# Kernel optimization log

Measured on AMD Instinct MI355X. Metric: run time of the kernel, lower is better.

## Reference

```python
import jax, jax.numpy as jnp
import numpy as np

N_NODES = 100000


def setup_inputs() -> dict:
    key = jax.random.key(0)
    k1, k2, k3 = jax.random.split(key, 3)
    feat = jax.random.normal(k1, (N_NODES, 64), dtype=jnp.float32)
    src = jax.random.randint(k2, (1250000,), 0, N_NODES, dtype=jnp.int64)
    dst = jax.random.randint(k3, (1250000,), 0, N_NODES, dtype=jnp.int64)
    return {"feat": feat, "src": src, "dst": dst}


def reference(feat, src, dst):
    # GraphConv(norm='both', activation=None): degree-normalized neighbor sum
    # with implicit self-connection (rst = feat_dst + sum_neighbors), where
    # degrees are clamp(min=1) + 1 to account for the self edge.
    n = feat.shape[0]
    ones = jnp.ones(src.shape[0], dtype=feat.dtype)
    out_deg = jax.ops.segment_sum(ones, src, num_segments=n)
    in_deg = jax.ops.segment_sum(ones, dst, num_segments=n)
    norm_l = jax.lax.rsqrt(jnp.maximum(out_deg, 1.0) + 1.0)  # [N]
    norm_r = jax.lax.rsqrt(jnp.maximum(in_deg, 1.0) + 1.0)   # [N]
    feat_src = feat * norm_l[:, None]                         # left-normalize
    msgs = feat_src[src]                                      # gather [E, D]
    h_neigh = jax.ops.segment_sum(msgs, dst, num_segments=n)  # scatter-sum [N, D]
    rst = (feat + h_neigh) * norm_r[:, None]                  # right-normalize
    return rst
```

## Files before the change

kernel.cpp:

```cpp
#include <hip/hip_runtime.h>


#define GC_D 64
#define PSIZE 196
#define SCAP 3072
#define EPT 12
#define EPB (512*EPT)
#define MAXPART 512
#define GC_CAP 64


__global__ __launch_bounds__(512) void partition_kernel(
        const int* __restrict__ src,
        const int* __restrict__ dst,
        int* __restrict__ curA,
        int* __restrict__ curB,
        int* __restrict__ streamA,
        unsigned char* __restrict__ streamB,
        int e, int nPart) {
    __shared__ int histA[MAXPART], histB[MAXPART], baseA[MAXPART], baseB[MAXPART];
    __shared__ int lofsA[MAXPART];
    __shared__ int sval[EPB];
    __shared__ unsigned short sbin[EPB];
    int t = threadIdx.x;
    for (int i = t; i < nPart; i += 512) { histA[i] = 0; histB[i] = 0; }
    __syncthreads();
    int lo = blockIdx.x * EPB;
    int base_i = lo + t * EPT;
    int se[EPT], de[EPT], rkA[EPT], rkB[EPT];
    bool aligned16 = ((((size_t)src) | ((size_t)dst)) & 15) == 0;
    if (aligned16 && base_i + EPT <= e) {
        int4 s0 = *(const int4*)(src + base_i);
        int4 s1 = *(const int4*)(src + base_i + 4);
        int4 s2 = *(const int4*)(src + base_i + 8);
        int4 d0 = *(const int4*)(dst + base_i);
        int4 d1 = *(const int4*)(dst + base_i + 4);
        int4 d2 = *(const int4*)(dst + base_i + 8);
        se[0]=s0.x; se[1]=s0.y; se[2]=s0.z; se[3]=s0.w;
        se[4]=s1.x; se[5]=s1.y; se[6]=s1.z; se[7]=s1.w;
        se[8]=s2.x; se[9]=s2.y; se[10]=s2.z; se[11]=s2.w;
        de[0]=d0.x; de[1]=d0.y; de[2]=d0.z; de[3]=d0.w;
        de[4]=d1.x; de[5]=d1.y; de[6]=d1.z; de[7]=d1.w;
        de[8]=d2.x; de[9]=d2.y; de[10]=d2.z; de[11]=d2.w;
#pragma unroll
        for (int k = 0; k < EPT; ++k) {
            rkA[k] = atomicAdd(&histA[de[k] / PSIZE], 1);
            rkB[k] = atomicAdd(&histB[se[k] / PSIZE], 1);
        }
    } else {
#pragma unroll
        for (int k = 0; k < EPT; ++k) {
            int i = base_i + k;
            se[k] = 0; de[k] = 0; rkA[k] = 0; rkB[k] = 0;
            if (i < e) {
                se[k] = src[i]; de[k] = dst[i];
                rkA[k] = atomicAdd(&histA[de[k] / PSIZE], 1);
                rkB[k] = atomicAdd(&histB[se[k] / PSIZE], 1);
            }
        }
    }
    __syncthreads();
    for (int i = t; i < nPart; i += 512) {
        int hA = histA[i];
        baseA[i] = hA ? atomicAdd(&curA[i], hA) : 0;
        int hB = histB[i];
        baseB[i] = hB ? atomicAdd(&curB[i], hB) : 0;
    }
    lofsA[t] = (t < nPart) ? histA[t] : 0;
    __syncthreads();
    for (int off = 1; off < MAXPART; off <<= 1) {
        int a = (t >= off) ? lofsA[t - off] : 0;
        __syncthreads();
        lofsA[t] += a;
        __syncthreads();
    }
#pragma unroll
    for (int k = 0; k < EPT; ++k) {
        int i = base_i + k;
        if (i < e) {
            int s = se[k], d = de[k];
            int pA = d / PSIZE;
            int slot = lofsA[pA] - histA[pA] + rkA[k];
            sval[slot] = s | ((d - pA * PSIZE) << 17);
            sbin[slot] = (unsigned short)pA;
            int pB = s / PSIZE;
            int posB = baseB[pB] + rkB[k];
            if (posB < SCAP) streamB[pB * SCAP + posB] = (unsigned char)(s - pB * PSIZE);
        }
    }
    __syncthreads();
    int nE = min(EPB, e - lo);
    for (int i = t; i < nE; i += 512) {
        int bin = sbin[i];
        int pos = baseA[bin] + (i - (lofsA[bin] - histA[bin]));
        if (pos < SCAP) streamA[bin * SCAP + pos] = sval[i];
    }
}

__device__ __forceinline__ unsigned short to_bf16_rne(float v) {
    unsigned b = __float_as_uint(v);
    b = (b + 0x7FFFu + ((b >> 16) & 1u)) >> 16;
    return (unsigned short)b;
}

__global__ __launch_bounds__(512) void convertB_kernel(
        const int* __restrict__ curB,
        const unsigned char* __restrict__ streamB,
        const float* __restrict__ feat,
        unsigned short* __restrict__ featb,
        int n) {
    __shared__ int lodeg[256];
    __shared__ float lnl[256];
    int p = blockIdx.x, t = threadIdx.x;
    if (t < 256) lodeg[t] = 0;
    __syncthreads();
    int cB = min(curB[p], SCAP);
    const unsigned char* sB = streamB + (size_t)p * SCAP;
    for (int i = t; i < cB; i += 512) atomicAdd(&lodeg[sB[i]], 1);
    __syncthreads();
    if (t < 256) lnl[t] = rsqrtf(fmaxf((float)lodeg[t], 1.0f) + 1.0f);
    __syncthreads();
    int g = p * PSIZE;
    for (int q = t; q < PSIZE * 16; q += 512) {
        int r = q >> 4;
        int node = g + r;
        if (node >= n) break;
        float nl = lnl[r];
        size_t base = (size_t)node * GC_D + (q & 15) * 4;
        const float4 v = *(const float4*)(feat + base);
        ushort4 rr;
        rr.x = to_bf16_rne(v.x * nl);
        rr.y = to_bf16_rne(v.y * nl);
        rr.z = to_bf16_rne(v.z * nl);
        rr.w = to_bf16_rne(v.w * nl);
        *(ushort4*)(featb + base) = rr;
    }
    if (p == 0 && t < GC_D) featb[(size_t)n * GC_D + t] = 0;
}

__global__ __launch_bounds__(1024) void sortgather_kernel(
        const int* __restrict__ curA,
        const int* __restrict__ streamA,
        const float* __restrict__ feat,
        const unsigned short* __restrict__ featb,
        float* __restrict__ out,
        int n) {
    __shared__ int lperm[SCAP];
    __shared__ int lcnt[256], loff[256];
    int p = blockIdx.x, t = threadIdx.x;
    if (t < 256) lcnt[t] = 0;
    __syncthreads();
    int cA = min(curA[p], SCAP);
    const int* sA = streamA + (size_t)p * SCAP;
    int vv[3], rk[3];
#pragma unroll
    for (int it = 0; it < 3; ++it) {
        int i = it * 1024 + t;
        vv[it] = 0; rk[it] = -1;
        if (i < cA) {
            int v = sA[i];
            vv[it] = v;
            rk[it] = atomicAdd(&lcnt[(v >> 17) & 255], 1);
        }
    }
    __syncthreads();
    if (t < 256) loff[t] = lcnt[t];
    __syncthreads();
    for (int off = 1; off < 256; off <<= 1) {
        int a = (t < 256 && t >= off) ? loff[t - off] : 0;
        __syncthreads();
        if (t < 256) loff[t] += a;
        __syncthreads();
    }
    if (t < 256) loff[t] -= lcnt[t];
    __syncthreads();
#pragma unroll
    for (int it = 0; it < 3; ++it) {
        if (rk[it] >= 0) {
            int v = vv[it];
            lperm[loff[(v >> 17) & 255] + rk[it]] = v & 0x1FFFF;
        }
    }
    __syncthreads();
    int wave = t >> 6, lane = t & 63;
    int half = lane >> 5;
    int c = lane & 31;
    int g = p * PSIZE;
    for (int r = wave; r < PSIZE; r += 16) {
        int node = g + r;
        if (node >= n) break;
        int deg = lcnt[r];
        int off = loff[r];
        float acc0 = 0.0f, acc1 = 0.0f;
        for (int base = 0; base < deg; base += 64) {
            int m = min(deg - base, 64);
            int s_l = (lane < m) ? lperm[off + base + lane] : n;
            int m16 = (m + 15) & ~15;
            for (int j = 0; j < m16; j += 16) {
#pragma unroll
                for (int k = 0; k < 8; ++k) {
                    int s = __shfl(s_l, j + 2 * k + half);
                    unsigned u = *(const unsigned*)(featb + (size_t)s * GC_D + 2 * c);
                    acc0 += __uint_as_float(u << 16);
                    acc1 += __uint_as_float(u & 0xFFFF0000u);
                }
            }
        }
        acc0 += __shfl_xor(acc0, 32);
        acc1 += __shfl_xor(acc1, 32);
        if (half == 0) {
            float nr = rsqrtf(fmaxf((float)deg, 1.0f) + 1.0f);
            const float2 self = *(const float2*)(feat + (size_t)node * GC_D + 2 * c);
            float2 rr;
            rr.x = (self.x + acc0) * nr;
            rr.y = (self.y + acc1) * nr;
            *(float2*)(out + (size_t)node * GC_D + 2 * c) = rr;
        }
    }
}


__global__ void zero_int_kernel(int* __restrict__ p, int n) {
    int i = blockIdx.x * blockDim.x + threadIdx.x;
    if (i < n) p[i] = 0;
}

__global__ void bucket_hist_kernel(const int* __restrict__ src,
                                   const int* __restrict__ dst,
                                   int* __restrict__ cnt,
                                   int* __restrict__ outdeg,
                                   int* __restrict__ bucket,
                                   int e) {
    int i = blockIdx.x * blockDim.x + threadIdx.x;
    if (i < e) {
        int s = src[i];
        int d = dst[i];
        atomicAdd(&outdeg[s], 1);
        int pos = atomicAdd(&cnt[d], 1);
        if (pos < GC_CAP) bucket[d * GC_CAP + pos] = s;
    }
}

__global__ __launch_bounds__(256) void convert_kernel(
        const float* __restrict__ feat,
        const int* __restrict__ outdeg,
        unsigned short* __restrict__ featb,
        int n) {
    int i = blockIdx.x * 256 + threadIdx.x;
    int row = i >> 4;
    if (row > n) return;
    if (row == n) {
        ushort4 z; z.x = 0; z.y = 0; z.z = 0; z.w = 0;
        *(ushort4*)(featb + (size_t)i * 4) = z;
        return;
    }
    float nl = rsqrtf(fmaxf((float)outdeg[row], 1.0f) + 1.0f);
    float4 v = *(const float4*)(feat + (size_t)i * 4);
    ushort4 r;
    r.x = to_bf16_rne(v.x * nl);
    r.y = to_bf16_rne(v.y * nl);
    r.z = to_bf16_rne(v.z * nl);
    r.w = to_bf16_rne(v.w * nl);
    *(ushort4*)(featb + (size_t)i * 4) = r;
}

__global__ __launch_bounds__(256) void gather_bf16_kernel(
        const float* __restrict__ feat,
        const unsigned short* __restrict__ featb,
        const int* __restrict__ bucket,
        const int* __restrict__ cnt,
        float* __restrict__ out,
        int n) {
    int wid = (blockIdx.x * blockDim.x + threadIdx.x) >> 6;
    int lane = threadIdx.x & 63;
    if (wid >= n) return;
    int deg = cnt[wid];
    int s_raw = bucket[wid * GC_CAP + lane];
    int m = min(deg, GC_CAP);
    int s_l = (lane < m) ? s_raw : n;
    int half = lane >> 5;
    int c = lane & 31;
    float acc0 = 0.0f, acc1 = 0.0f;
    int m16 = (m + 15) & ~15;
    for (int j = 0; j < m16; j += 16) {
#pragma unroll
        for (int k = 0; k < 8; ++k) {
            int s = __shfl(s_l, j + 2 * k + half);
            unsigned u = *(const unsigned*)(featb + (size_t)s * GC_D + 2 * c);
            acc0 += __uint_as_float(u << 16);
            acc1 += __uint_as_float(u & 0xFFFF0000u);
        }
    }
    acc0 += __shfl_xor(acc0, 32);
    acc1 += __shfl_xor(acc1, 32);
    if (half == 0) {
        float nr = rsqrtf(fmaxf((float)deg, 1.0f) + 1.0f);
        const float2 self = *(const float2*)(feat + (size_t)wid * GC_D + 2 * c);
        float2 r;
        r.x = (self.x + acc0) * nr;
        r.y = (self.y + acc1) * nr;
        *(float2*)(out + (size_t)wid * GC_D + 2 * c) = r;
    }
}


extern "C" void kernel_launch(void* const* d_in, const int* in_sizes, int n_in,
                              void* d_out, int out_size, void* d_ws, size_t ws_size,
                              hipStream_t stream) {
    const float* feat = (const float*)d_in[0];
    const int*   src  = (const int*)d_in[1];
    const int*   dst  = (const int*)d_in[2];
    float* out = (float*)d_out;

    const int n = in_sizes[0] / GC_D;
    const int e = in_sizes[1];
    const int nPart = (n + PSIZE - 1) / PSIZE;

    size_t featb_ints = ((size_t)(n + 1) * GC_D + 1) / 2;
    size_t o = 2 * (size_t)nPart;
    o = (o + 31) & ~(size_t)31;
    size_t streamA_o = o;  o += (size_t)nPart * SCAP;
    size_t featb_o = o;    o += featb_ints;
    size_t need_main = o * sizeof(int) + (size_t)nPart * SCAP;

    size_t featb_bytes = (size_t)(n + 1) * GC_D * sizeof(unsigned short);
    size_t need_bf16 = ((size_t)2 * n + (size_t)n * GC_CAP) * sizeof(int) + featb_bytes;

    bool main_ok = (ws_size >= need_main) && nPart <= MAXPART && n <= 131071;

    if (main_ok) {
        int* ws = (int*)d_ws;
        int* curA = ws;
        int* curB = ws + nPart;
        int* streamA = ws + streamA_o;
        unsigned short* featb = (unsigned short*)(ws + featb_o);
        unsigned char* streamB = (unsigned char*)(ws + o);

        hipMemsetAsync(curA, 0, 2 * (size_t)nPart * sizeof(int), stream);
        partition_kernel<<<(e + EPB - 1) / EPB, 512, 0, stream>>>(
            src, dst, curA, curB, streamA, streamB, e, nPart);
        convertB_kernel<<<nPart, 512, 0, stream>>>(curB, streamB, feat, featb, n);
        sortgather_kernel<<<nPart, 1024, 0, stream>>>(curA, streamA, feat, featb,
                                                      out, n);
    } else if (ws_size >= need_bf16) {
        int* cnt    = (int*)d_ws;
        int* outdeg = cnt + n;
        int* bucket = outdeg + n;
        unsigned short* featb = (unsigned short*)(bucket + (size_t)n * GC_CAP);

        zero_int_kernel<<<(2 * n + 255) / 256, 256, 0, stream>>>(cnt, 2 * n);
        bucket_hist_kernel<<<(e + 255) / 256, 256, 0, stream>>>(src, dst, cnt,
                                                                outdeg, bucket, e);
        int conv_threads = (n + 1) * 16;
        convert_kernel<<<(conv_threads + 255) / 256, 256, 0, stream>>>(
            feat, outdeg, featb, n);
        long long total = (long long)n * GC_D;
        gather_bf16_kernel<<<(int)((total + 255) / 256), 256, 0, stream>>>(
            feat, featb, bucket, cnt, out, n);
    }
}
```

Measured before the change: 139.8 us.

## Split bf16 feature table into four column slabs for cache-local gathers

Stores the normalized bf16 features as four slabs of 16 columns (32 bytes per node) instead of interleaved 128-byte rows. The gather kernel loops over slabs, so each pass touches a table a quarter the size, which is meant to fit better in L2/MALL. Each wave now handles 8 edges per load step with 8 lanes per edge. The cost is re-reading the edge permutation four times, narrower 32-byte gathers, and a longer shuffle reduction.

```diff
diff --git a/kernel.cpp b/kernel.cpp
--- a/kernel.cpp
+++ b/kernel.cpp
@@ -121,21 +121,26 @@
     if (t < 256) lnl[t] = rsqrtf(fmaxf((float)lodeg[t], 1.0f) + 1.0f);
     __syncthreads();
     int g = p * PSIZE;
+    const size_t slabStride = (size_t)(n + 1) * 16;
     for (int q = t; q < PSIZE * 16; q += 512) {
         int r = q >> 4;
         int node = g + r;
         if (node >= n) break;
         float nl = lnl[r];
-        size_t base = (size_t)node * GC_D + (q & 15) * 4;
-        const float4 v = *(const float4*)(feat + base);
+        int quad = q & 15;
+        const float4 v = *(const float4*)(feat + (size_t)node * GC_D + quad * 4);
         ushort4 rr;
         rr.x = to_bf16_rne(v.x * nl);
         rr.y = to_bf16_rne(v.y * nl);
         rr.z = to_bf16_rne(v.z * nl);
         rr.w = to_bf16_rne(v.w * nl);
-        *(ushort4*)(featb + base) = rr;
-    }
-    if (p == 0 && t < GC_D) featb[(size_t)n * GC_D + t] = 0;
+        *(ushort4*)(featb + (size_t)(quad >> 2) * slabStride
+                    + (size_t)node * 16 + (quad & 3) * 4) = rr;
+    }
+    if (p == 0 && t < GC_D) {
+        int s = t >> 4, col = t & 15;
+        featb[(size_t)s * slabStride + (size_t)n * 16 + col] = 0;
+    }
 }
 
 __global__ __launch_bounds__(1024) void sortgather_kernel(
@@ -183,38 +188,41 @@
     }
     __syncthreads();
     int wave = t >> 6, lane = t & 63;
-    int half = lane >> 5;
-    int c = lane & 31;
+    int eg = lane >> 3;
+    int cp = lane & 7;
     int g = p * PSIZE;
-    for (int r = wave; r < PSIZE; r += 16) {
-        int node = g + r;
-        if (node >= n) break;
-        int deg = lcnt[r];
-        int off = loff[r];
-        float acc0 = 0.0f, acc1 = 0.0f;
-        for (int base = 0; base < deg; base += 64) {
-            int m = min(deg - base, 64);
-            int s_l = (lane < m) ? lperm[off + base + lane] : n;
-            int m16 = (m + 15) & ~15;
-            for (int j = 0; j < m16; j += 16) {
-#pragma unroll
-                for (int k = 0; k < 8; ++k) {
-                    int s = __shfl(s_l, j + 2 * k + half);
-                    unsigned u = *(const unsigned*)(featb + (size_t)s * GC_D + 2 * c);
+    const size_t slabStride = (size_t)(n + 1) * 16;
+    for (int slab = 0; slab < 4; ++slab) {
+        const unsigned short* fb = featb + (size_t)slab * slabStride;
+        int cbase = slab * 16 + 2 * cp;
+        for (int r = wave; r < PSIZE; r += 16) {
+            int node = g + r;
+            if (node >= n) break;
+            int deg = lcnt[r];
+            int off = loff[r];
+            float acc0 = 0.0f, acc1 = 0.0f;
+            for (int base = 0; base < deg; base += 64) {
+                int m = min(deg - base, 64);
+                int s_l = (lane < m) ? lperm[off + base + lane] : n;
+                int m8 = (m + 7) & ~7;
+                for (int j = 0; j < m8; j += 8) {
+                    int s = __shfl(s_l, j + eg);
+                    unsigned u = *(const unsigned*)(fb + (size_t)s * 16 + 2 * cp);
                     acc0 += __uint_as_float(u << 16);
                     acc1 += __uint_as_float(u & 0xFFFF0000u);
                 }
             }
-        }
-        acc0 += __shfl_xor(acc0, 32);
-        acc1 += __shfl_xor(acc1, 32);
-        if (half == 0) {
-            float nr = rsqrtf(fmaxf((float)deg, 1.0f) + 1.0f);
-            const float2 self = *(const float2*)(feat + (size_t)node * GC_D + 2 * c);
-            float2 rr;
-            rr.x = (self.x + acc0) * nr;
-            rr.y = (self.y + acc1) * nr;
-            *(float2*)(out + (size_t)node * GC_D + 2 * c) = rr;
+            acc0 += __shfl_xor(acc0, 8);  acc1 += __shfl_xor(acc1, 8);
+            acc0 += __shfl_xor(acc0, 16); acc1 += __shfl_xor(acc1, 16);
+            acc0 += __shfl_xor(acc0, 32); acc1 += __shfl_xor(acc1, 32);
+            if (eg == 0) {
+                float nr = rsqrtf(fmaxf((float)deg, 1.0f) + 1.0f);
+                const float2 self = *(const float2*)(feat + (size_t)node * GC_D + cbase);
+                float2 rr;
+                rr.x = (self.x + acc0) * nr;
+                rr.y = (self.y + acc1) * nr;
+                *(float2*)(out + (size_t)node * GC_D + cbase) = rr;
+            }
         }
     }
 }
```

Measured after the change: 189.9 us. 1.36x slower.
